# Performance work log

Hardware: AMD Instinct MI355X
Metric: run time of the kernel (lower is better)

The kernel has to match this reference:

```python
import jax, jax.numpy as jnp
import numpy as np

NUM_CLASSES = 2
THRESHOLD = 0.35   # overlap_thresh
NEG_POS = 7        # negative:positive mining ratio
VAR0, VAR1 = 0.1, 0.2  # self.variance


def point_form(boxes):
    # (cx,cy,w,h) -> (xmin,ymin,xmax,ymax); boxes [P,4]
    return jnp.concatenate([boxes[:, :2] - boxes[:, 2:] / 2,
                            boxes[:, :2] + boxes[:, 2:] / 2], axis=1)


def jaccard(box_a, box_b):
    # box_a [B,O,4] xyxy, box_b [P,4] xyxy -> IoU [B,O,P]
    max_xy = jnp.minimum(box_a[:, :, None, 2:], box_b[None, None, :, 2:])
    min_xy = jnp.maximum(box_a[:, :, None, :2], box_b[None, None, :, :2])
    wh = jnp.clip(max_xy - min_xy, 0.0)
    inter = wh[..., 0] * wh[..., 1]
    area_a = ((box_a[..., 2] - box_a[..., 0]) * (box_a[..., 3] - box_a[..., 1]))[:, :, None]
    area_b = ((box_b[:, 2] - box_b[:, 0]) * (box_b[:, 3] - box_b[:, 1]))[None, None, :]
    return inter / (area_a + area_b - inter)


def encode(matched, priors):
    # matched [B,P,4] xyxy, priors [1,P,4] cxcywh -> offsets [B,P,4]
    g_cxcy = (matched[..., :2] + matched[..., 2:]) / 2 - priors[..., :2]
    g_cxcy = g_cxcy / (VAR0 * priors[..., 2:])
    g_wh = (matched[..., 2:] - matched[..., :2]) / priors[..., 2:]
    g_wh = jnp.log(g_wh) / VAR1
    return jnp.concatenate([g_cxcy, g_wh], axis=-1)


def match(truths, labels, priors):
    # truths [B,O,4] xyxy, labels [B,O] float, priors [P,4] cxcywh
    overlaps = jaccard(truths, point_form(priors))      # [B,O,P]
    best_prior_idx = jnp.argmax(overlaps, axis=2)       # [B,O] best prior per gt
    best_truth_overlap = jnp.max(overlaps, axis=1)      # [B,P]
    best_truth_idx = jnp.argmax(overlaps, axis=1)       # [B,P] best gt per prior
    O = truths.shape[1]

    def fix(bto, bti, bpi):
        # ensure every gt keeps its best prior (index_fill_ / loop in torch)
        bto = bto.at[bpi].set(2.0)
        bti = bti.at[bpi].set(jnp.arange(O))
        return bto, bti

    best_truth_overlap, best_truth_idx = jax.vmap(fix)(
        best_truth_overlap, best_truth_idx, best_prior_idx)
    matched = jnp.take_along_axis(truths, best_truth_idx[..., None], axis=1)  # [B,P,4]
    conf = jnp.take_along_axis(labels, best_truth_idx, axis=1).astype(jnp.int32) + 1
    conf = jnp.where(best_truth_overlap < THRESHOLD, 0, conf)  # background
    loc = encode(matched, priors[None])
    return loc, conf


def setup_inputs() -> dict:
    key = jax.random.key(0)
    k1, k2, k3, k4, k5, k6 = jax.random.split(key, 6)
    B, P, O, C = 32, 32768, 32, NUM_CLASSES
    loc_data = jax.random.normal(k1, (B, P, 4), jnp.float32)
    conf_data = jax.random.normal(k2, (B, P, C), jnp.float32)
    # priors: (cx,cy,w,h) in [0,1], wh in [0.02,0.3]
    p_cxcy = jax.random.uniform(k3, (P, 2), jnp.float32)
    p_wh = 0.02 + 0.28 * jax.random.uniform(k4, (P, 2), jnp.float32)
    priors = jnp.concatenate([p_cxcy, p_wh], axis=1)
    # targets: valid xyxy boxes + label column (label 0 -> class 1 after +1)
    t_cxcy = 0.1 + 0.8 * jax.random.uniform(k5, (B, O, 2), jnp.float32)
    t_wh = 0.05 + 0.2 * jax.random.uniform(k6, (B, O, 2), jnp.float32)
    boxes = jnp.concatenate([t_cxcy - t_wh / 2, t_cxcy + t_wh / 2], axis=2)
    labels = jnp.zeros((B, O, 1), jnp.float32)
    targets = jnp.concatenate([boxes, labels], axis=2)
    return {"loc_data": loc_data, "conf_data": conf_data,
            "priors": priors, "targets": targets}


def reference(loc_data, conf_data, priors, targets):
    B, P, C = conf_data.shape
    truths = targets[..., :4]
    labels = targets[..., 4]
    loc_t, conf_t = match(truths, labels, priors)   # [B,P,4], [B,P] int
    pos = conf_t > 0                                # [B,P]

    # localization: smooth-L1 summed over positives
    diff = loc_data - loc_t
    ad = jnp.abs(diff)
    sl1 = jnp.where(ad < 1.0, 0.5 * diff * diff, ad - 0.5)
    loss_l = jnp.sum(sl1 * pos[..., None].astype(loc_data.dtype))

    # per-prior CE loss for hard-negative mining
    lse = jax.nn.logsumexp(conf_data, axis=2)                            # [B,P]
    picked = jnp.take_along_axis(conf_data, conf_t[..., None], axis=2)[..., 0]
    ce = lse - picked                                                    # [B,P]
    mine = jnp.where(pos, 0.0, ce)
    # double-argsort rank trick (descending)
    loss_idx = jnp.argsort(-mine, axis=1)
    idx_rank = jnp.argsort(loss_idx, axis=1)
    num_pos = jnp.sum(pos, axis=1, keepdims=True)                        # [B,1]
    num_neg = jnp.minimum(NEG_POS * num_pos, P - 1)
    neg = idx_rank < num_neg

    sel = pos | neg
    loss_c = jnp.sum(jnp.where(sel, ce, 0.0))

    N = jnp.maximum(jnp.sum(num_pos).astype(jnp.float32), 1.0)
    return loss_l / N, loss_c / N
```

## Files before the change

### kernel.cpp

```cpp
#include <hip/hip_runtime.h>
#include <stdint.h>

#define NB 32
#define NP 32768
#define NO 32
#define THRESH 0.35f

typedef unsigned long long u64;
typedef unsigned int u32;

__device__ __forceinline__ float iou_corners(float px1, float py1, float px2, float py2, float ab,
                                             float tx1, float ty1, float tx2, float ty2, float aa)
{
#pragma clang fp contract(off)
    float iw = fminf(tx2, px2) - fmaxf(tx1, px1);
    float ih = fminf(ty2, py2) - fmaxf(ty1, py1);
    iw = fmaxf(iw, 0.f); ih = fmaxf(ih, 0.f);
    float inter = iw * ih;
    return __fdividef(inter, aa + ab - inter);
}

__device__ __forceinline__ float smooth_l1_sum(float4 ld, float4 pr, float4 tt)
{
#pragma clang fp contract(off)
    float g0 = __fdividef((tt.x + tt.z) * 0.5f - pr.x, 0.1f * pr.z);
    float g1 = __fdividef((tt.y + tt.w) * 0.5f - pr.y, 0.1f * pr.w);
    float g2 = __logf(__fdividef(tt.z - tt.x, pr.z)) * 5.0f;
    float g3 = __logf(__fdividef(tt.w - tt.y, pr.w)) * 5.0f;
    float d0 = ld.x - g0, d1 = ld.y - g1, d2 = ld.z - g2, d3 = ld.w - g3;
    float a0 = fabsf(d0), a1 = fabsf(d1), a2 = fabsf(d2), a3 = fabsf(d3);
    return (a0 < 1.f ? 0.5f * d0 * d0 : a0 - 0.5f)
         + (a1 < 1.f ? 0.5f * d1 * d1 : a1 - 0.5f)
         + (a2 < 1.f ? 0.5f * d2 * d2 : a2 - 0.5f)
         + (a3 < 1.f ? 0.5f * d3 * d3 : a3 - 0.5f);
}

__device__ __forceinline__ float lse2(float c0, float c1)
{
#pragma clang fp contract(off)
    float mm = fmaxf(c0, c1), mn = fminf(c0, c1);
    return mm + __logf(1.f + __expf(mn - mm));
}

__global__ __launch_bounds__(256) void kern1(
        const float* __restrict__ loc, const float* __restrict__ conf,
        const float* __restrict__ priors, const float* __restrict__ targets,
        float* __restrict__ mine, u64* __restrict__ bpk_part,
        float* __restrict__ part_sl1, float* __restrict__ part_cep, int* __restrict__ part_np,
        float* __restrict__ sl_tot, float* __restrict__ c_tot,
        int* __restrict__ np_tot, int* __restrict__ done_cnt)
{
#pragma clang fp contract(off)
    __shared__ __align__(16) float4 tbc[NO];
    __shared__ float ta[NO], tlab[NO];
    __shared__ u64 keys[NO];
    __shared__ float rs0[4], rs1[4];
    __shared__ int rc[4];
    const int b = blockIdx.y, x = blockIdx.x, tid = threadIdx.x;
    if (b == 0 && x == 0 && tid == 0) {
        *sl_tot = 0.f; *c_tot = 0.f; *np_tot = 0; *done_cnt = 0;
    }
    if (tid < NO * 5) {
        int o = tid / 5, c = tid % 5;
        float v = targets[b * NO * 5 + tid];
        if (c < 4) ((float*)&tbc[o])[c] = v; else tlab[o] = v;
    }
    if (tid < NO) keys[tid] = 0ull;
    __syncthreads();
    if (tid < NO) {
        float4 t = tbc[tid];
        ta[tid] = (t.z - t.x) * (t.w - t.y);
    }
    __syncthreads();

    const int p0 = x * 1024 + tid * 4;
    float4 pr[4];
    float px1[4], py1[4], px2[4], py2[4], ab[4];
#pragma unroll
    for (int j = 0; j < 4; ++j) {
        pr[j] = ((const float4*)priors)[p0 + j];
        px1[j] = pr[j].x - pr[j].z * 0.5f;
        py1[j] = pr[j].y - pr[j].w * 0.5f;
        px2[j] = pr[j].x + pr[j].z * 0.5f;
        py2[j] = pr[j].y + pr[j].w * 0.5f;
        ab[j]  = pr[j].z * pr[j].w;
    }
    u64 bk[4] = {0ull, 0ull, 0ull, 0ull};
    const int lane_o = tid & 31;
    for (int it = 0; it < NO; ++it) {
        const int o = (it + lane_o) & 31;
        float4 tt = tbc[o];
        float aa = ta[o];
        float iou4[4];
#pragma unroll
        for (int j = 0; j < 4; ++j) {
            float iou = iou_corners(px1[j], py1[j], px2[j], py2[j], ab[j],
                                    tt.x, tt.y, tt.z, tt.w, aa);
            iou4[j] = iou;
            u64 ko = ((u64)__float_as_uint(iou) << 6) | (u64)(63 - o);
            bk[j] = bk[j] > ko ? bk[j] : ko;
        }
        float vm = fmaxf(fmaxf(iou4[0], iou4[1]), fmaxf(iou4[2], iou4[3]));
        u64 cur = keys[o];
        if (__float_as_uint(vm) > (u32)(cur >> 32)) {
            float bi = iou4[3]; int bp = p0 + 3;
            if (iou4[2] >= bi) { bi = iou4[2]; bp = p0 + 2; }
            if (iou4[1] >= bi) { bi = iou4[1]; bp = p0 + 1; }
            if (iou4[0] >= bi) { bi = iou4[0]; bp = p0 + 0; }
            atomicMax(&keys[o], ((u64)__float_as_uint(bi) << 32) | (u64)(~(u32)bp));
        }
    }

    const size_t gbase = (size_t)b * NP + p0;
    float4 cfa = ((const float4*)conf)[gbase / 2];
    float4 cfb = ((const float4*)conf)[gbase / 2 + 1];
    float c0[4] = {cfa.x, cfa.z, cfb.x, cfb.z};
    float c1[4] = {cfa.y, cfa.w, cfb.y, cfb.w};
    float4 mout;
    float s_sl1 = 0.f, s_cep = 0.f;
    int np = 0;
#pragma unroll
    for (int j = 0; j < 4; ++j) {
        u32 vb = (u32)(bk[j] >> 6);
        float bv = __uint_as_float(vb);
        int o = 63 - (int)(bk[j] & 63);
        int cf = (bv < THRESH) ? 0 : ((int)tlab[o] + 1);
        bool pos = cf > 0;
        float4 ld = ((const float4*)loc)[gbase + j];
        float sl1 = smooth_l1_sum(ld, pr[j], tbc[o]);
        float ce = lse2(c0[j], c1[j]) - ((cf == 0) ? c0[j] : c1[j]);
        if (pos) { s_sl1 += sl1; s_cep += ce; np++; }
        ((float*)&mout)[j] = pos ? 0.f : ce;
    }
    ((float4*)mine)[gbase / 4] = mout;

#pragma unroll
    for (int m = 32; m; m >>= 1) {
        s_sl1 += __shfl_xor(s_sl1, m, 64);
        s_cep += __shfl_xor(s_cep, m, 64);
        np    += __shfl_xor(np, m, 64);
    }
    int lane = tid & 63, w = tid >> 6;
    if (lane == 0) { rs0[w] = s_sl1; rs1[w] = s_cep; rc[w] = np; }
    __syncthreads();
    if (tid == 0) {
        float t0 = 0.f, t1 = 0.f; int t2 = 0;
        for (int i = 0; i < 4; ++i) { t0 += rs0[i]; t1 += rs1[i]; t2 += rc[i]; }
        part_sl1[b * 32 + x] = t0;
        part_cep[b * 32 + x] = t1;
        part_np [b * 32 + x] = t2;
    }
    if (tid < NO) bpk_part[(b * 32 + x) * 32 + tid] = keys[tid];
}

#define HCOL 65
__global__ __launch_bounds__(1024) void kern3(
        const float* __restrict__ loc, const float* __restrict__ conf,
        const float* __restrict__ priors, const float* __restrict__ targets,
        const u64* __restrict__ bpk_part, const float* __restrict__ mine,
        const float* __restrict__ part_sl1, const float* __restrict__ part_cep,
        const int* __restrict__ part_np,
        float* __restrict__ sl_tot, float* __restrict__ c_tot,
        int* __restrict__ np_tot, int* __restrict__ done_cnt,
        float* __restrict__ out)
{
#pragma clang fp contract(off)
    const int b = blockIdx.x, tid = threadIdx.x;
    const int wave = tid >> 6, lane = tid & 63;
    __shared__ __align__(16) float4 tbc[NO];
    __shared__ float tlab[NO], tas[NO];
    __shared__ u32 pp[NO];
    __shared__ u32 flags[1024];
    __shared__ int hist[256 * HCOL];
    __shared__ int total[256];
    __shared__ float rs[16];
    __shared__ int rc2[16];
    __shared__ float sh_sl1, sh_cep;
    __shared__ int sh_np, sh_k, sh_kk;
    __shared__ u32 sh_prefix;

    if (tid < NO * 5) {
        int o = tid / 5, c = tid % 5;
        float v = targets[b * NO * 5 + tid];
        if (c < 4) ((float*)&tbc[o])[c] = v; else tlab[o] = v;
    }
    flags[tid] = 0u;

    const float* mb = mine + (size_t)b * NP;
    float v[32];
#pragma unroll
    for (int q = 0; q < 8; ++q) {
        float4 t4 = ((const float4*)mb)[q * 1024 + tid];
        v[4 * q] = t4.x; v[4 * q + 1] = t4.y; v[4 * q + 2] = t4.z; v[4 * q + 3] = t4.w;
    }
    __syncthreads();
    if (tid < NO) {
        float4 t = tbc[tid];
        tas[tid] = (t.z - t.x) * (t.w - t.y);
        u64 key = 0ull;
        for (int xx = 0; xx < 32; ++xx) {
            u64 t2 = bpk_part[(b * 32 + xx) * 32 + tid];
            key = t2 > key ? t2 : key;
        }
        pp[tid] = (key >> 32) ? ~(u32)key : 0u;
    }
    __syncthreads();
    if (tid < NO) {
        const int o = tid;
        const u32 p = pp[o];
        float dsl1 = 0.f, dcep = 0.f; int dnp = 0;
        bool last = true;
        for (int o2 = o + 1; o2 < NO; ++o2)
            if (pp[o2] == p) { last = false; break; }
        if (last) {
            float4 prr = ((const float4*)priors)[p];
            float px1 = prr.x - prr.z * 0.5f, py1 = prr.y - prr.w * 0.5f;
            float px2 = prr.x + prr.z * 0.5f, py2 = prr.y + prr.w * 0.5f;
            float ab = prr.z * prr.w;
            float bv = -1.f; int bo_ = 0;
            for (int o2 = 0; o2 < NO; ++o2) {
                float4 t2 = tbc[o2];
                float i2 = iou_corners(px1, py1, px2, py2, ab, t2.x, t2.y, t2.z, t2.w, tas[o2]);
                if (i2 > bv) { bv = i2; bo_ = o2; }
            }
            int cf_pre = (bv < THRESH) ? 0 : ((int)tlab[bo_] + 1);
            size_t gp = (size_t)b * NP + p;
            float4 ld = ((const float4*)loc)[gp];
            float2 c = ((const float2*)conf)[gp];
            float lse = lse2(c.x, c.y);
            int cf_new = (int)tlab[o] + 1;
            dsl1 = smooth_l1_sum(ld, prr, tbc[o]);
            dcep = lse - ((cf_new == 0) ? c.x : c.y);
            dnp = 1;
            if (cf_pre > 0) {
                dsl1 -= smooth_l1_sum(ld, prr, tbc[bo_]);
                dcep -= lse - ((cf_pre == 0) ? c.x : c.y);
                dnp = 0;
            }
            atomicOr(&flags[p >> 5], 1u << (p & 31));
        }
        float a = part_sl1[b * 32 + o] + dsl1;
        float d = part_cep[b * 32 + o] + dcep;
        int   n = part_np [b * 32 + o] + dnp;
#pragma unroll
        for (int m = 16; m; m >>= 1) {
            a += __shfl_xor(a, m, 32);
            d += __shfl_xor(d, m, 32);
            n += __shfl_xor(n, m, 32);
        }
        if (o == 0) {
            sh_sl1 = a; sh_cep = d; sh_np = n;
            sh_k = min(7 * n, NP - 1); sh_kk = sh_k; sh_prefix = 0u;
        }
    }
    __syncthreads();
#pragma unroll
    for (int q = 0; q < 8; ++q) {
        u32 word = flags[q * 128 + (tid >> 3)];
#pragma unroll
        for (int c = 0; c < 4; ++c)
            if ((word >> (((tid & 7) << 2) + c)) & 1u) v[4 * q + c] = 0.f;
    }
    const int k = sh_k;
    float topk = 0.f;
    if (k > 0) {
        for (int pass = 0; pass < 4; ++pass) {
            for (int i = tid; i < 256 * HCOL; i += 1024) hist[i] = 0;
            __syncthreads();
            const int shift = 24 - 8 * pass;
            const u32 pfx = sh_prefix;
#pragma unroll 8
            for (int j = 0; j < 32; ++j) {
                u32 kb = __float_as_uint(v[j]);
                if ((u32)(((u64)kb) >> (shift + 8)) == pfx)
                    atomicAdd(&hist[((kb >> shift) & 255) * HCOL + lane], 1);
            }
            __syncthreads();
            {
                int bin = tid >> 2, q = tid & 3;
                const int base = bin * HCOL + q * 16;
                int s = 0;
#pragma unroll
                for (int i = 0; i < 16; ++i) s += hist[base + i];
                s += __shfl_xor(s, 2, 64);
                s += __shfl_xor(s, 1, 64);
                if (q == 0) total[bin] = s;
            }
            __syncthreads();
            if (tid < 64) {
                int4 h4 = ((const int4*)total)[tid];
                int s3 = h4.w, s2 = h4.z + s3, s1 = h4.y + s2, s0 = h4.x + s1;
                int acc = s0;
#pragma unroll
                for (int off = 1; off < 64; off <<= 1) {
                    int u = __shfl_down(acc, off, 64);
                    if (tid + off < 64) acc += u;
                }
                int excl = acc - s0;
                int kk = sh_kk;
                int cand = -1, nkk = 0;
                if (excl + s3 >= kk)      { cand = 4 * tid + 3; nkk = kk - excl; }
                else if (excl + s2 >= kk) { cand = 4 * tid + 2; nkk = kk - excl - s3; }
                else if (excl + s1 >= kk) { cand = 4 * tid + 1; nkk = kk - excl - s2; }
                else if (excl + s0 >= kk) { cand = 4 * tid + 0; nkk = kk - excl - s1; }
                int cmax = cand;
#pragma unroll
                for (int off = 1; off < 64; off <<= 1) cmax = max(cmax, __shfl_xor(cmax, off, 64));
                if (cand >= 0 && cand == cmax) {
                    sh_prefix = (pfx << 8) | (u32)(cand & 255);
                    sh_kk = nkk;
                }
            }
            __syncthreads();
        }
        const u32 T = sh_prefix;
        const float tval = __uint_as_float(T);
        float s = 0.f; int c2 = 0;
#pragma unroll
        for (int j = 0; j < 32; ++j) {
            if (__float_as_uint(v[j]) > T) { s += v[j]; c2++; }
        }
#pragma unroll
        for (int m = 32; m; m >>= 1) {
            s  += __shfl_xor(s, m, 64);
            c2 += __shfl_xor(c2, m, 64);
        }
        if (lane == 0) { rs[wave] = s; rc2[wave] = c2; }
        __syncthreads();
        if (tid == 0) {
            float st = 0.f; int ct = 0;
            for (int i = 0; i < 16; ++i) { st += rs[i]; ct += rc2[i]; }
            topk = st + (float)(k - ct) * tval;
        }
    }
    if (tid == 0) {
        atomicAdd(sl_tot, sh_sl1);
        atomicAdd(c_tot, sh_cep + topk);
        atomicAdd(np_tot, sh_np);
        __threadfence();
        int d = atomicAdd(done_cnt, 1);
        if (d == NB - 1) {
            float sl = atomicAdd(sl_tot, 0.f);
            float cc = atomicAdd(c_tot, 0.f);
            int   np = atomicAdd(np_tot, 0);
            float N = fmaxf((float)np, 1.f);
            out[0] = sl / N;
            out[1] = cc / N;
        }
    }
}

extern "C" void kernel_launch(void* const* d_in, const int* in_sizes, int n_in,
                              void* d_out, int out_size, void* d_ws, size_t ws_size,
                              hipStream_t stream) {
    const float* loc     = (const float*)d_in[0];
    const float* conf    = (const float*)d_in[1];
    const float* priors  = (const float*)d_in[2];
    const float* targets = (const float*)d_in[3];
    float* out = (float*)d_out;

    char* ws = (char*)d_ws;
    float* mine     = (float*)ws;
    u64*   bpk_part = (u64*)(ws + 4194304);
    float* part_sl1 = (float*)(ws + 4456448);
    float* part_cep = (float*)(ws + 4460544);
    int*   part_np  = (int*)(ws + 4464640);
    float* sl_tot   = (float*)(ws + 4468736);
    float* c_tot    = (float*)(ws + 4468740);
    int*   np_tot   = (int*)(ws + 4468744);
    int*   done_cnt = (int*)(ws + 4468748);

    dim3 g1(32, NB);
    kern1<<<g1, 256, 0, stream>>>(loc, conf, priors, targets, mine, bpk_part,
                                  part_sl1, part_cep, part_np,
                                  sl_tot, c_tot, np_tot, done_cnt);
    kern3<<<NB, 1024, 0, stream>>>(loc, conf, priors, targets, bpk_part, mine,
                                   part_sl1, part_cep, part_np,
                                   sl_tot, c_tot, np_tot, done_cnt, out);
}
```

Measured before the change: 136.5 us.

## Double kern1 grid and build first radix histogram before match fixups

```diff
diff --git a/kernel.cpp b/kernel.cpp
--- a/kernel.cpp
+++ b/kernel.cpp
@@ -5,6 +5,7 @@
 #define NP 32768
 #define NO 32
 #define THRESH 0.35f
+#define NT1 64
 
 typedef unsigned long long u64;
 typedef unsigned int u32;
@@ -73,11 +74,11 @@
     }
     __syncthreads();
 
-    const int p0 = x * 1024 + tid * 4;
-    float4 pr[4];
-    float px1[4], py1[4], px2[4], py2[4], ab[4];
-#pragma unroll
-    for (int j = 0; j < 4; ++j) {
+    const int p0 = x * 512 + tid * 2;
+    float4 pr[2];
+    float px1[2], py1[2], px2[2], py2[2], ab[2];
+#pragma unroll
+    for (int j = 0; j < 2; ++j) {
         pr[j] = ((const float4*)priors)[p0 + j];
         px1[j] = pr[j].x - pr[j].z * 0.5f;
         py1[j] = pr[j].y - pr[j].w * 0.5f;
@@ -85,54 +86,51 @@
         py2[j] = pr[j].y + pr[j].w * 0.5f;
         ab[j]  = pr[j].z * pr[j].w;
     }
-    u64 bk[4] = {0ull, 0ull, 0ull, 0ull};
+    u64 bk[2] = {0ull, 0ull};
     const int lane_o = tid & 31;
     for (int it = 0; it < NO; ++it) {
         const int o = (it + lane_o) & 31;
         float4 tt = tbc[o];
         float aa = ta[o];
-        float iou4[4];
-#pragma unroll
-        for (int j = 0; j < 4; ++j) {
+        float iou2[2];
+#pragma unroll
+        for (int j = 0; j < 2; ++j) {
             float iou = iou_corners(px1[j], py1[j], px2[j], py2[j], ab[j],
                                     tt.x, tt.y, tt.z, tt.w, aa);
-            iou4[j] = iou;
+            iou2[j] = iou;
             u64 ko = ((u64)__float_as_uint(iou) << 6) | (u64)(63 - o);
             bk[j] = bk[j] > ko ? bk[j] : ko;
         }
-        float vm = fmaxf(fmaxf(iou4[0], iou4[1]), fmaxf(iou4[2], iou4[3]));
+        float vm = fmaxf(iou2[0], iou2[1]);
         u64 cur = keys[o];
         if (__float_as_uint(vm) > (u32)(cur >> 32)) {
-            float bi = iou4[3]; int bp = p0 + 3;
-            if (iou4[2] >= bi) { bi = iou4[2]; bp = p0 + 2; }
-            if (iou4[1] >= bi) { bi = iou4[1]; bp = p0 + 1; }
-            if (iou4[0] >= bi) { bi = iou4[0]; bp = p0 + 0; }
+            float bi = iou2[1]; int bp = p0 + 1;
+            if (iou2[0] >= bi) { bi = iou2[0]; bp = p0; }
             atomicMax(&keys[o], ((u64)__float_as_uint(bi) << 32) | (u64)(~(u32)bp));
         }
     }
 
     const size_t gbase = (size_t)b * NP + p0;
-    float4 cfa = ((const float4*)conf)[gbase / 2];
-    float4 cfb = ((const float4*)conf)[gbase / 2 + 1];
-    float c0[4] = {cfa.x, cfa.z, cfb.x, cfb.z};
-    float c1[4] = {cfa.y, cfa.w, cfb.y, cfb.w};
-    float4 mout;
+    float4 cf = ((const float4*)conf)[gbase >> 1];
+    float c0[2] = {cf.x, cf.z};
+    float c1[2] = {cf.y, cf.w};
+    float2 mout;
     float s_sl1 = 0.f, s_cep = 0.f;
     int np = 0;
 #pragma unroll
-    for (int j = 0; j < 4; ++j) {
+    for (int j = 0; j < 2; ++j) {
         u32 vb = (u32)(bk[j] >> 6);
         float bv = __uint_as_float(vb);
         int o = 63 - (int)(bk[j] & 63);
-        int cf = (bv < THRESH) ? 0 : ((int)tlab[o] + 1);
-        bool pos = cf > 0;
+        int cfv = (bv < THRESH) ? 0 : ((int)tlab[o] + 1);
+        bool pos = cfv > 0;
         float4 ld = ((const float4*)loc)[gbase + j];
         float sl1 = smooth_l1_sum(ld, pr[j], tbc[o]);
-        float ce = lse2(c0[j], c1[j]) - ((cf == 0) ? c0[j] : c1[j]);
+        float ce = lse2(c0[j], c1[j]) - ((cfv == 0) ? c0[j] : c1[j]);
         if (pos) { s_sl1 += sl1; s_cep += ce; np++; }
         ((float*)&mout)[j] = pos ? 0.f : ce;
     }
-    ((float4*)mine)[gbase / 4] = mout;
+    ((float2*)mine)[gbase >> 1] = mout;
 
 #pragma unroll
     for (int m = 32; m; m >>= 1) {
@@ -146,14 +144,14 @@
     if (tid == 0) {
         float t0 = 0.f, t1 = 0.f; int t2 = 0;
         for (int i = 0; i < 4; ++i) { t0 += rs0[i]; t1 += rs1[i]; t2 += rc[i]; }
-        part_sl1[b * 32 + x] = t0;
-        part_cep[b * 32 + x] = t1;
-        part_np [b * 32 + x] = t2;
-    }
-    if (tid < NO) bpk_part[(b * 32 + x) * 32 + tid] = keys[tid];
-}
-
-#define HCOL 65
+        part_sl1[b * NT1 + x] = t0;
+        part_cep[b * NT1 + x] = t1;
+        part_np [b * NT1 + x] = t2;
+    }
+    if (tid < NO) bpk_part[(b * NT1 + x) * 32 + tid] = keys[tid];
+}
+
+#define HCOL 33
 __global__ __launch_bounds__(1024) void kern3(
         const float* __restrict__ loc, const float* __restrict__ conf,
         const float* __restrict__ priors, const float* __restrict__ targets,
@@ -167,6 +165,7 @@
 #pragma clang fp contract(off)
     const int b = blockIdx.x, tid = threadIdx.x;
     const int wave = tid >> 6, lane = tid & 63;
+    const int cl = lane & 31;
     __shared__ __align__(16) float4 tbc[NO];
     __shared__ float tlab[NO], tas[NO];
     __shared__ u32 pp[NO];
@@ -185,6 +184,7 @@
         if (c < 4) ((float*)&tbc[o])[c] = v; else tlab[o] = v;
     }
     flags[tid] = 0u;
+    for (int i = tid; i < 256 * HCOL; i += 1024) hist[i] = 0;
 
     const float* mb = mine + (size_t)b * NP;
     float v[32];
@@ -194,12 +194,15 @@
         v[4 * q] = t4.x; v[4 * q + 1] = t4.y; v[4 * q + 2] = t4.z; v[4 * q + 3] = t4.w;
     }
     __syncthreads();
+#pragma unroll 8
+    for (int j = 0; j < 32; ++j)
+        atomicAdd(&hist[(__float_as_uint(v[j]) >> 24) * HCOL + cl], 1);
     if (tid < NO) {
         float4 t = tbc[tid];
         tas[tid] = (t.z - t.x) * (t.w - t.y);
         u64 key = 0ull;
-        for (int xx = 0; xx < 32; ++xx) {
-            u64 t2 = bpk_part[(b * 32 + xx) * 32 + tid];
+        for (int xx = 0; xx < NT1; ++xx) {
+            u64 t2 = bpk_part[(b * NT1 + xx) * 32 + tid];
             key = t2 > key ? t2 : key;
         }
         pp[tid] = (key >> 32) ? ~(u32)key : 0u;
@@ -237,11 +240,14 @@
                 dcep -= lse - ((cf_pre == 0) ? c.x : c.y);
                 dnp = 0;
             }
+            float oldv = mb[p];
+            atomicSub(&hist[(__float_as_uint(oldv) >> 24) * HCOL + cl], 1);
+            atomicAdd(&hist[cl], 1);
             atomicOr(&flags[p >> 5], 1u << (p & 31));
         }
-        float a = part_sl1[b * 32 + o] + dsl1;
-        float d = part_cep[b * 32 + o] + dcep;
-        int   n = part_np [b * 32 + o] + dnp;
+        float a = part_sl1[b * NT1 + o] + part_sl1[b * NT1 + 32 + o] + dsl1;
+        float d = part_cep[b * NT1 + o] + part_cep[b * NT1 + 32 + o] + dcep;
+        int   n = part_np [b * NT1 + o] + part_np [b * NT1 + 32 + o] + dnp;
 #pragma unroll
         for (int m = 16; m; m >>= 1) {
             a += __shfl_xor(a, m, 32);
@@ -265,26 +271,27 @@
     float topk = 0.f;
     if (k > 0) {
         for (int pass = 0; pass < 4; ++pass) {
-            for (int i = tid; i < 256 * HCOL; i += 1024) hist[i] = 0;
-            __syncthreads();
-            const int shift = 24 - 8 * pass;
-            const u32 pfx = sh_prefix;
+            if (pass > 0) {
+                for (int i = tid; i < 256 * HCOL; i += 1024) hist[i] = 0;
+                __syncthreads();
+                const int shift = 24 - 8 * pass;
+                const u32 pfx = sh_prefix;
 #pragma unroll 8
-            for (int j = 0; j < 32; ++j) {
-                u32 kb = __float_as_uint(v[j]);
-                if ((u32)(((u64)kb) >> (shift + 8)) == pfx)
-                    atomicAdd(&hist[((kb >> shift) & 255) * HCOL + lane], 1);
-            }
-            __syncthreads();
-            {
-                int bin = tid >> 2, q = tid & 3;
-                const int base = bin * HCOL + q * 16;
+                for (int j = 0; j < 32; ++j) {
+                    u32 kb = __float_as_uint(v[j]);
+                    if ((u32)(((u64)kb) >> (shift + 8)) == pfx)
+                        atomicAdd(&hist[((kb >> shift) & 255) * HCOL + cl], 1);
+                }
+                __syncthreads();
+            }
+            if (tid < 512) {
+                int bin = tid >> 1;
+                const int base = bin * HCOL + (tid & 1) * 16;
                 int s = 0;
 #pragma unroll
                 for (int i = 0; i < 16; ++i) s += hist[base + i];
-                s += __shfl_xor(s, 2, 64);
                 s += __shfl_xor(s, 1, 64);
-                if (q == 0) total[bin] = s;
+                if ((tid & 1) == 0) total[bin] = s;
             }
             __syncthreads();
             if (tid < 64) {
@@ -307,7 +314,7 @@
 #pragma unroll
                 for (int off = 1; off < 64; off <<= 1) cmax = max(cmax, __shfl_xor(cmax, off, 64));
                 if (cand >= 0 && cand == cmax) {
-                    sh_prefix = (pfx << 8) | (u32)(cand & 255);
+                    sh_prefix = (sh_prefix << 8) | (u32)(cand & 255);
                     sh_kk = nkk;
                 }
             }
@@ -362,15 +369,15 @@
     char* ws = (char*)d_ws;
     float* mine     = (float*)ws;
     u64*   bpk_part = (u64*)(ws + 4194304);
-    float* part_sl1 = (float*)(ws + 4456448);
-    float* part_cep = (float*)(ws + 4460544);
-    int*   part_np  = (int*)(ws + 4464640);
-    float* sl_tot   = (float*)(ws + 4468736);
-    float* c_tot    = (float*)(ws + 4468740);
-    int*   np_tot   = (int*)(ws + 4468744);
-    int*   done_cnt = (int*)(ws + 4468748);
-
-    dim3 g1(32, NB);
+    float* part_sl1 = (float*)(ws + 4718592);
+    float* part_cep = (float*)(ws + 4726784);
+    int*   part_np  = (int*)(ws + 4734976);
+    float* sl_tot   = (float*)(ws + 4743168);
+    float* c_tot    = (float*)(ws + 4743172);
+    int*   np_tot   = (int*)(ws + 4743176);
+    int*   done_cnt = (int*)(ws + 4743180);
+
+    dim3 g1(NT1, NB);
     kern1<<<g1, 256, 0, stream>>>(loc, conf, priors, targets, mine, bpk_part,
                                   part_sl1, part_cep, part_np,
                                   sl_tot, c_tot, np_tot, done_cnt);
```

New measurement: 127.2 us. 6.9% less time.
